# Kernel tuning notes

Measured on AMD Instinct MI355X. Metric: run time of the kernel, lower is better.

## Reference

```python
import jax, jax.numpy as jnp
import numpy as np

NUM_HASH_BUCKETS = 9311
OUT_CHANNELS = 64
B, C, L = 8192, 32, 8


def setup_inputs() -> dict:
    key = jax.random.key(0)
    k_x, k_emb = jax.random.split(key)
    x = jax.random.randint(k_x, (B, C, L), 0, NUM_HASH_BUCKETS, dtype=jnp.int64)
    emb_table = jax.random.normal(k_emb, (NUM_HASH_BUCKETS, OUT_CHANNELS), dtype=jnp.float32)
    # padding_idx=0 -> row 0 is zeros
    emb_table = emb_table.at[0].set(0.0)
    return {"x": x, "emb_table": emb_table}


def reference(x, emb_table):
    # x: [B, C, L] int64 category ids (0 = padding)
    num_buckets = emb_table.shape[0]
    x = jnp.maximum(x, 0)                      # relu (faithful to float branch; ints already >= 0)
    hashed = x % num_buckets                   # hash -> bucket id
    emb = emb_table[hashed]                    # gather: [B, C, L, D]
    mask = (x > 0).astype(emb.dtype)[..., None]  # [B, C, L, 1]
    sum_emb = jnp.sum(emb * mask, axis=2)      # [B, C, D]
    counts = jnp.maximum(jnp.sum(mask, axis=2), 1.0)  # [B, C, 1]
    return sum_emb / counts
```

## Files before the change

### kernel.cpp

```cpp
#include <hip/hip_runtime.h>


#define NPAIRS (8192 * 32)
#define LL 8
#define NROWS 9311
#define D 64
#define TAB_ELEMS (NROWS * D)
#define HALF_PAIRS (NPAIRS / 2)

typedef float  vfloat4 __attribute__((ext_vector_type(4)));
typedef int    vint4   __attribute__((ext_vector_type(4)));
typedef unsigned int  uint32;
typedef unsigned int  vuint4 __attribute__((ext_vector_type(4)));
typedef unsigned short vushort4 __attribute__((ext_vector_type(4)));

__global__ __launch_bounds__(256) void
cvt_table_bf16(const vfloat4* __restrict__ src, vushort4* __restrict__ dst, int n4) {
    const int i = blockIdx.x * blockDim.x + threadIdx.x;
    if (i >= n4) return;
    const vfloat4 f = src[i];
    vushort4 o;
    #pragma unroll
    for (int k = 0; k < 4; ++k) {
        uint32 b = __float_as_uint(f[k]);
        b = (b + 0x7fff + ((b >> 16) & 1)) >> 16;
        o[k] = (unsigned short)b;
    }
    dst[i] = o;
}

__global__ __launch_bounds__(256) void
SharedMultiCategoricalEncoder_kernel(const int* __restrict__ x,
                                     const vuint4* __restrict__ tab,
                                     vfloat4* __restrict__ out4) {
    const int tid   = blockIdx.x * blockDim.x + threadIdx.x;
    const int pairA = tid >> 3;
    const int pairB = pairA + HALF_PAIRS;
    const int sub   = tid & 7;

    const vint4* xpA = (const vint4*)(x + pairA * LL);
    const vint4* xpB = (const vint4*)(x + pairB * LL);
    const vint4 a01 = xpA[0];
    const vint4 a23 = xpA[1];
    const vint4 b01 = xpB[0];
    const vint4 b23 = xpB[1];
    const int idsA[LL] = { a01.x, a01.y, a01.z, a01.w, a23.x, a23.y, a23.z, a23.w };
    const int idsB[LL] = { b01.x, b01.y, b01.z, b01.w, b23.x, b23.y, b23.z, b23.w };

    vuint4 eA[LL], eB[LL];
#pragma unroll
    for (int l = 0; l < LL; ++l) eA[l] = tab[idsA[l] * 8 + sub];
#pragma unroll
    for (int l = 0; l < LL; ++l) eB[l] = tab[idsB[l] * 8 + sub];

    float accA[8] = {0.f}, accB[8] = {0.f};
    int cntA = 0, cntB = 0;
#pragma unroll
    for (int l = 0; l < LL; ++l) {
        #pragma unroll
        for (int k = 0; k < 4; ++k) {
            const uint32 ua = eA[l][k];
            accA[2*k]   += __uint_as_float(ua << 16);
            accA[2*k+1] += __uint_as_float(ua & 0xffff0000u);
            const uint32 ub = eB[l][k];
            accB[2*k]   += __uint_as_float(ub << 16);
            accB[2*k+1] += __uint_as_float(ub & 0xffff0000u);
        }
        cntA += (idsA[l] > 0);
        cntB += (idsB[l] > 0);
    }

    const float sA = 1.0f / (float)(cntA > 0 ? cntA : 1);
    const float sB = 1.0f / (float)(cntB > 0 ? cntB : 1);

    vfloat4* opA = out4 + pairA * 16 + sub * 2;
    vfloat4* opB = out4 + pairB * 16 + sub * 2;
    opA[0] = (vfloat4){accA[0], accA[1], accA[2], accA[3]} * sA;
    opA[1] = (vfloat4){accA[4], accA[5], accA[6], accA[7]} * sA;
    opB[0] = (vfloat4){accB[0], accB[1], accB[2], accB[3]} * sB;
    opB[1] = (vfloat4){accB[4], accB[5], accB[6], accB[7]} * sB;
}

extern "C" void kernel_launch(void* const* d_in, const int* in_sizes, int n_in,
                              void* d_out, int out_size, void* d_ws, size_t ws_size,
                              hipStream_t stream) {
    const int*   x   = (const int*)d_in[0];
    const float* emb = (const float*)d_in[1];
    float*       out = (float*)d_out;

    const int n4 = TAB_ELEMS / 4;
    cvt_table_bf16<<<(n4 + 255) / 256, 256, 0, stream>>>(
        (const vfloat4*)emb, (vushort4*)d_ws, n4);

    const int threads = 256;
    const int blocks  = (HALF_PAIRS * 8) / threads;
    SharedMultiCategoricalEncoder_kernel<<<blocks, threads, 0, stream>>>(
        x, (const vuint4*)d_ws, (vfloat4*)out);
}
```

Before: 94.24 us.

## Gather fp32 table directly and drop bf16 conversion pre-pass

Removes the separate kernel that converted the embedding table to bf16 and gathers fp32 rows directly, with 16 threads per (b,c) pair each reading one float4. This eliminates a kernel launch and a table-conversion pass and restores full precision, at the cost of doubling gather bytes per row and doubling the thread count. Index loads and output stores now use nontemporal hints to avoid polluting cache with streaming data.

Result: slower. 107.5 us (+14.0%).

```diff
diff --git a/kernel.cpp b/kernel.cpp
--- a/kernel.cpp
+++ b/kernel.cpp
@@ -5,67 +5,42 @@
 #define LL 8
 #define NROWS 9311
 #define D 64
-#define TAB_ELEMS (NROWS * D)
 #define HALF_PAIRS (NPAIRS / 2)
 
 typedef float  vfloat4 __attribute__((ext_vector_type(4)));
 typedef int    vint4   __attribute__((ext_vector_type(4)));
-typedef unsigned int  uint32;
-typedef unsigned int  vuint4 __attribute__((ext_vector_type(4)));
-typedef unsigned short vushort4 __attribute__((ext_vector_type(4)));
-
-__global__ __launch_bounds__(256) void
-cvt_table_bf16(const vfloat4* __restrict__ src, vushort4* __restrict__ dst, int n4) {
-    const int i = blockIdx.x * blockDim.x + threadIdx.x;
-    if (i >= n4) return;
-    const vfloat4 f = src[i];
-    vushort4 o;
-    #pragma unroll
-    for (int k = 0; k < 4; ++k) {
-        uint32 b = __float_as_uint(f[k]);
-        b = (b + 0x7fff + ((b >> 16) & 1)) >> 16;
-        o[k] = (unsigned short)b;
-    }
-    dst[i] = o;
-}
 
 __global__ __launch_bounds__(256) void
 SharedMultiCategoricalEncoder_kernel(const int* __restrict__ x,
-                                     const vuint4* __restrict__ tab,
+                                     const vfloat4* __restrict__ tab4,
                                      vfloat4* __restrict__ out4) {
     const int tid   = blockIdx.x * blockDim.x + threadIdx.x;
-    const int pairA = tid >> 3;
+    const int pairA = tid >> 4;
     const int pairB = pairA + HALF_PAIRS;
-    const int sub   = tid & 7;
+    const int sub   = tid & 15;
 
     const vint4* xpA = (const vint4*)(x + pairA * LL);
     const vint4* xpB = (const vint4*)(x + pairB * LL);
-    const vint4 a01 = xpA[0];
-    const vint4 a23 = xpA[1];
-    const vint4 b01 = xpB[0];
-    const vint4 b23 = xpB[1];
+    const vint4 a01 = __builtin_nontemporal_load(xpA);
+    const vint4 a23 = __builtin_nontemporal_load(xpA + 1);
+    const vint4 b01 = __builtin_nontemporal_load(xpB);
+    const vint4 b23 = __builtin_nontemporal_load(xpB + 1);
     const int idsA[LL] = { a01.x, a01.y, a01.z, a01.w, a23.x, a23.y, a23.z, a23.w };
     const int idsB[LL] = { b01.x, b01.y, b01.z, b01.w, b23.x, b23.y, b23.z, b23.w };
 
-    vuint4 eA[LL], eB[LL];
+    vfloat4 gA[LL], gB[LL];
 #pragma unroll
-    for (int l = 0; l < LL; ++l) eA[l] = tab[idsA[l] * 8 + sub];
+    for (int l = 0; l < LL; ++l) gA[l] = tab4[idsA[l] * 16 + sub];
 #pragma unroll
-    for (int l = 0; l < LL; ++l) eB[l] = tab[idsB[l] * 8 + sub];
+    for (int l = 0; l < LL; ++l) gB[l] = tab4[idsB[l] * 16 + sub];
 
-    float accA[8] = {0.f}, accB[8] = {0.f};
+    vfloat4 accA = {0.f, 0.f, 0.f, 0.f};
+    vfloat4 accB = {0.f, 0.f, 0.f, 0.f};
     int cntA = 0, cntB = 0;
 #pragma unroll
     for (int l = 0; l < LL; ++l) {
-        #pragma unroll
-        for (int k = 0; k < 4; ++k) {
-            const uint32 ua = eA[l][k];
-            accA[2*k]   += __uint_as_float(ua << 16);
-            accA[2*k+1] += __uint_as_float(ua & 0xffff0000u);
-            const uint32 ub = eB[l][k];
-            accB[2*k]   += __uint_as_float(ub << 16);
-            accB[2*k+1] += __uint_as_float(ub & 0xffff0000u);
-        }
+        accA += gA[l];
+        accB += gB[l];
         cntA += (idsA[l] > 0);
         cntB += (idsB[l] > 0);
     }
@@ -73,12 +48,8 @@
     const float sA = 1.0f / (float)(cntA > 0 ? cntA : 1);
     const float sB = 1.0f / (float)(cntB > 0 ? cntB : 1);
 
-    vfloat4* opA = out4 + pairA * 16 + sub * 2;
-    vfloat4* opB = out4 + pairB * 16 + sub * 2;
-    opA[0] = (vfloat4){accA[0], accA[1], accA[2], accA[3]} * sA;
-    opA[1] = (vfloat4){accA[4], accA[5], accA[6], accA[7]} * sA;
-    opB[0] = (vfloat4){accB[0], accB[1], accB[2], accB[3]} * sB;
-    opB[1] = (vfloat4){accB[4], accB[5], accB[6], accB[7]} * sB;
+    __builtin_nontemporal_store(accA * sA, out4 + pairA * 16 + sub);
+    __builtin_nontemporal_store(accB * sB, out4 + pairB * 16 + sub);
 }
 
 extern "C" void kernel_launch(void* const* d_in, const int* in_sizes, int n_in,
@@ -88,12 +59,10 @@
     const float* emb = (const float*)d_in[1];
     float*       out = (float*)d_out;
 
-    const int n4 = TAB_ELEMS / 4;
-    cvt_table_bf16<<<(n4 + 255) / 256, 256, 0, stream>>>(
-        (const vfloat4*)emb, (vushort4*)d_ws, n4);
+    (void)d_ws; (void)ws_size;
 
     const int threads = 256;
-    const int blocks  = (HALF_PAIRS * 8) / threads;
+    const int blocks  = (HALF_PAIRS * 16) / threads;
     SharedMultiCategoricalEncoder_kernel<<<blocks, threads, 0, stream>>>(
-        x, (const vuint4*)d_ws, (vfloat4*)out);
+        x, (const vfloat4*)emb, (vfloat4*)out);
 }
```
